# Performance work log

Measured on AMD Instinct MI355X. Metric: run time of the kernel, lower is better.

Reference implementation:

```python
import jax, jax.numpy as jnp
import numpy as np

N_NODES = 4096
EMB_DIM = 512
N_HEADS = 8
K_SPARSE = 128
HEAD_DIM = EMB_DIM // N_HEADS


def setup_inputs() -> dict:
    key = jax.random.key(0)
    k1, k2, k3, k4 = jax.random.split(key, 4)
    # xavier_uniform bound for square [D, D] weight
    bound = float(np.sqrt(6.0 / (EMB_DIM + EMB_DIM)))
    return {
        "embedding_matrix": jax.random.normal(k1, (N_NODES, EMB_DIM), dtype=jnp.float32),
        "Wq": jax.random.uniform(k2, (EMB_DIM, EMB_DIM), minval=-bound, maxval=bound, dtype=jnp.float32),
        "bq": jnp.zeros((EMB_DIM,), dtype=jnp.float32),
        "Wk": jax.random.uniform(k3, (EMB_DIM, EMB_DIM), minval=-bound, maxval=bound, dtype=jnp.float32),
        "bk": jnp.zeros((EMB_DIM,), dtype=jnp.float32),
        "sparse_indices": jax.random.randint(k4, (N_HEADS, N_NODES, K_SPARSE), 0, N_NODES, dtype=jnp.int32),
    }


def reference(embedding_matrix, Wq, bq, Wk, bk, sparse_indices):
    N, D = embedding_matrix.shape
    H, _, K = sparse_indices.shape
    hd = D // H
    # torch Linear: y = x @ W.T + b
    q = (embedding_matrix @ Wq.T + bq).reshape(N, H, hd).transpose(1, 0, 2)  # [H, N, hd]
    kk = (embedding_matrix @ Wk.T + bk).reshape(N, H, hd).transpose(1, 0, 2)  # [H, N, hd]
    # per-head gather of K random keys per query node: [H, N, K, hd]
    sel = jax.vmap(lambda kh, ih: kh[ih])(kk, sparse_indices)
    scores = jnp.einsum("hnd,hnkd->hnk", q, sel) / jnp.sqrt(jnp.float32(hd))  # [H, N, K]
    h_idx = jnp.arange(H)[:, None, None]
    n_idx = jnp.arange(N)[None, :, None]
    out = jnp.zeros((H, N, N), dtype=scores.dtype).at[h_idx, n_idx, sparse_indices].set(scores)
    return out
```

## Files before the change

kernel.cpp:

```cpp
#include <hip/hip_runtime.h>
#include <hip/hip_bf16.h>
#include <stdint.h>

#define N_NODES  4096
#define EMB_DIM  512
#define N_HEADS  8
#define K_SPARSE 128
#define HEAD_DIM 64

typedef __attribute__((ext_vector_type(8))) __bf16 bf16x8;
typedef __attribute__((ext_vector_type(4))) float  f32x4;

__device__ __forceinline__ float bf2f(unsigned short u) {
    union { unsigned int i; float f; } v;
    v.i = ((unsigned int)u) << 16;
    return v.f;
}

__device__ __forceinline__ unsigned short f2bf(float f) {
    union { float f; unsigned int i; } v;
    v.f = f;
    unsigned int x = v.i;
    unsigned int rounding = 0x7fffu + ((x >> 16) & 1u);
    x += rounding;
    return (unsigned short)(x >> 16);
}

__global__ __launch_bounds__(256) void proj_kernel(
    const float* __restrict__ X,
    const float* __restrict__ Wq, const float* __restrict__ bq,
    const float* __restrict__ Wk, const float* __restrict__ bk,
    unsigned short* __restrict__ Qb, unsigned short* __restrict__ Kb)
{
    __shared__ unsigned short As[64][40];
    __shared__ unsigned short Bs[128][40];

    const float* __restrict__ W    = blockIdx.z ? Wk : Wq;
    const float* __restrict__ bias = blockIdx.z ? bk : bq;
    unsigned short* __restrict__ out = blockIdx.z ? Kb : Qb;

    const int t    = threadIdx.x;
    const int M0   = blockIdx.x * 64;
    const int N0   = blockIdx.y * 128;
    const int lane = t & 63;
    const int wave = t >> 6;
    const int wm   = (wave >> 1) * 32;
    const int wn   = (wave & 1) * 64;

    const int arow = t >> 2;
    const int acol = (t & 3) * 8;
    const int brow = t >> 1;
    const int bcol = (t & 1) * 16;

    f32x4 acc[2][4] = {};

    for (int kt = 0; kt < EMB_DIM / 32; ++kt) {
        const int k0 = kt * 32;
        {
            const float4* srcA = (const float4*)(X + (size_t)(M0 + arow) * EMB_DIM + k0 + acol);
            float4 va0 = srcA[0], va1 = srcA[1];
            unsigned int pa[4];
            pa[0] = (unsigned int)f2bf(va0.x) | ((unsigned int)f2bf(va0.y) << 16);
            pa[1] = (unsigned int)f2bf(va0.z) | ((unsigned int)f2bf(va0.w) << 16);
            pa[2] = (unsigned int)f2bf(va1.x) | ((unsigned int)f2bf(va1.y) << 16);
            pa[3] = (unsigned int)f2bf(va1.z) | ((unsigned int)f2bf(va1.w) << 16);
            *(uint4*)&As[arow][acol] = make_uint4(pa[0], pa[1], pa[2], pa[3]);

            const float4* srcB = (const float4*)(W + (size_t)(N0 + brow) * EMB_DIM + k0 + bcol);
            unsigned int pb[8];
            #pragma unroll
            for (int c = 0; c < 4; ++c) {
                float4 vb = srcB[c];
                pb[c * 2 + 0] = (unsigned int)f2bf(vb.x) | ((unsigned int)f2bf(vb.y) << 16);
                pb[c * 2 + 1] = (unsigned int)f2bf(vb.z) | ((unsigned int)f2bf(vb.w) << 16);
            }
            uint4* dstB = (uint4*)&Bs[brow][bcol];
            dstB[0] = make_uint4(pb[0], pb[1], pb[2], pb[3]);
            dstB[1] = make_uint4(pb[4], pb[5], pb[6], pb[7]);
        }
        __syncthreads();

        bf16x8 af[2], bff[4];
        #pragma unroll
        for (int i = 0; i < 2; ++i)
            af[i] = __builtin_bit_cast(bf16x8,
                *(const uint4*)&As[wm + i * 16 + (lane & 15)][(lane >> 4) * 8]);
        #pragma unroll
        for (int i = 0; i < 4; ++i)
            bff[i] = __builtin_bit_cast(bf16x8,
                *(const uint4*)&Bs[wn + i * 16 + (lane & 15)][(lane >> 4) * 8]);

        #pragma unroll
        for (int mi = 0; mi < 2; ++mi)
            #pragma unroll
            for (int ni = 0; ni < 4; ++ni)
                acc[mi][ni] = __builtin_amdgcn_mfma_f32_16x16x32_bf16(
                    af[mi], bff[ni], acc[mi][ni], 0, 0, 0);
        __syncthreads();
    }

    #pragma unroll
    for (int mi = 0; mi < 2; ++mi) {
        #pragma unroll
        for (int ni = 0; ni < 4; ++ni) {
            const int col = N0 + wn + ni * 16 + (lane & 15);
            const float bval = bias[col];
            #pragma unroll
            for (int r = 0; r < 4; ++r) {
                const int row = M0 + wm + mi * 16 + (lane >> 4) * 4 + r;
                out[(size_t)row * EMB_DIM + col] = f2bf(acc[mi][ni][r] + bval);
            }
        }
    }
}

__global__ __launch_bounds__(64) void scatter_kernel(
    const unsigned short* __restrict__ Qb,
    const unsigned short* __restrict__ Kb,
    const int* __restrict__ sidx,
    float* __restrict__ out)
{
    __shared__ float rowbuf[N_NODES];

    const int t = threadIdx.x;
    const int b = blockIdx.x;
    const int h = b >> 12;
    const int n = b & (N_NODES - 1);
    const int j = t & 7;
    const int g = t >> 3;

    const int myIdx0 = sidx[(size_t)b * K_SPARSE + t];
    const int myIdx1 = sidx[(size_t)b * K_SPARSE + 64 + t];
    const uint4 qu = *(const uint4*)(Qb + (size_t)n * EMB_DIM + h * HEAD_DIM + j * 8);

    f32x4* rowv = (f32x4*)rowbuf;
    const f32x4 z4 = {0.0f, 0.0f, 0.0f, 0.0f};
    #pragma unroll
    for (int i = 0; i < 16; ++i) rowv[t + 64 * i] = z4;

    float q[8];
    {
        unsigned int uu[4] = {qu.x, qu.y, qu.z, qu.w};
        #pragma unroll
        for (int w = 0; w < 4; ++w) {
            q[2 * w + 0] = bf2f((unsigned short)(uu[w] & 0xffffu));
            q[2 * w + 1] = bf2f((unsigned short)(uu[w] >> 16));
        }
    }

    unsigned int* tags = (unsigned int*)rowbuf;
    asm volatile("s_waitcnt lgkmcnt(0)" ::: "memory");
    atomicMax(&tags[myIdx0], (unsigned int)(t + 1));
    atomicMax(&tags[myIdx1], (unsigned int)(t + 65));

    float score[16];
    int   kidx[16];
    #pragma unroll
    for (int p = 0; p < 16; ++p) {
        const int kk  = g + 8 * p;
        const int idx = (p < 8) ? __shfl(myIdx0, kk) : __shfl(myIdx1, kk - 64);
        kidx[p] = idx;
        const uint4 u = *(const uint4*)(Kb + (size_t)idx * EMB_DIM + h * HEAD_DIM + j * 8);
        unsigned int uu[4] = {u.x, u.y, u.z, u.w};
        float acc = 0.0f;
        #pragma unroll
        for (int w = 0; w < 4; ++w) {
            acc += bf2f((unsigned short)(uu[w] & 0xffffu)) * q[2 * w + 0];
            acc += bf2f((unsigned short)(uu[w] >> 16))     * q[2 * w + 1];
        }
        acc += __shfl_xor(acc, 1);
        acc += __shfl_xor(acc, 2);
        acc += __shfl_xor(acc, 4);
        score[p] = acc * 0.125f;
    }

    asm volatile("s_waitcnt lgkmcnt(0)" ::: "memory");
    if (j == 0) {
        unsigned int winmask = 0;
        #pragma unroll
        for (int p = 0; p < 16; ++p)
            if (tags[kidx[p]] == (unsigned int)(g + 8 * p + 1)) winmask |= (1u << p);
        asm volatile("s_waitcnt lgkmcnt(0)" ::: "memory");
        #pragma unroll
        for (int p = 0; p < 16; ++p)
            if (winmask & (1u << p)) rowbuf[kidx[p]] = score[p];
    }
    asm volatile("s_waitcnt lgkmcnt(0)" ::: "memory");

    f32x4* orowv = (f32x4*)(out + (size_t)b * N_NODES);
    #pragma unroll
    for (int i = 0; i < 16; ++i) {
        f32x4 v = rowv[t + 64 * i];
        __builtin_nontemporal_store(v, &orowv[t + 64 * i]);
    }
}

extern "C" void kernel_launch(void* const* d_in, const int* in_sizes, int n_in,
                              void* d_out, int out_size, void* d_ws, size_t ws_size,
                              hipStream_t stream) {
    const float* emb = (const float*)d_in[0];
    const float* Wq  = (const float*)d_in[1];
    const float* bq  = (const float*)d_in[2];
    const float* Wk  = (const float*)d_in[3];
    const float* bk  = (const float*)d_in[4];
    const int*   si  = (const int*)d_in[5];
    float* out = (float*)d_out;

    unsigned short* Qb = (unsigned short*)d_ws;
    unsigned short* Kb = Qb + (size_t)N_NODES * EMB_DIM;

    dim3 pg(N_NODES / 64, EMB_DIM / 128, 2);
    proj_kernel<<<pg, 256, 0, stream>>>(emb, Wq, bq, Wk, bk, Qb, Kb);

    scatter_kernel<<<N_HEADS * N_NODES, 64, 0, stream>>>(Qb, Kb, si, out);
}
```

Before: 579.6 us.

## Make scatter kernel persistent over 16 rows with software-pipelined gathers

The scatter kernel now uses 256-thread blocks that each process 16 consecutive output rows in a loop, instead of one 64-thread block per row. Key gathers and the index and query loads for the next rows are prefetched while the current row is written out, so load latency overlaps with the row stores. This cuts launch and scheduling overhead and hides gather latency. In exchange it adds several block-wide barriers per row, and each row's LDS zero/fill/readback is serialized within the block, which can reduce parallelism.

Result: slower. 620.1 us (+7.0%).

```diff
diff --git a/kernel.cpp b/kernel.cpp
--- a/kernel.cpp
+++ b/kernel.cpp
@@ -7,6 +7,9 @@
 #define N_HEADS  8
 #define K_SPARSE 128
 #define HEAD_DIM 64
+
+#define ROWS_PER_BLOCK 16
+#define SCATTER_BLOCKS (N_HEADS * N_NODES / ROWS_PER_BLOCK)
 
 typedef __attribute__((ext_vector_type(8))) __bf16 bf16x8;
 typedef __attribute__((ext_vector_type(4))) float  f32x4;
@@ -24,6 +27,12 @@
     unsigned int rounding = 0x7fffu + ((x >> 16) & 1u);
     x += rounding;
     return (unsigned short)(x >> 16);
+}
+
+__device__ __forceinline__ void lds_barrier() {
+    asm volatile("s_waitcnt lgkmcnt(0)" ::: "memory");
+    __builtin_amdgcn_s_barrier();
+    asm volatile("" ::: "memory");
 }
 
 __global__ __launch_bounds__(256) void proj_kernel(
@@ -114,84 +123,139 @@
     }
 }
 
-__global__ __launch_bounds__(64) void scatter_kernel(
+__global__ __launch_bounds__(256, 6) void scatter_kernel(
     const unsigned short* __restrict__ Qb,
     const unsigned short* __restrict__ Kb,
     const int* __restrict__ sidx,
     float* __restrict__ out)
 {
     __shared__ float rowbuf[N_NODES];
+    __shared__ int   sIdx[K_SPARSE];
 
     const int t = threadIdx.x;
-    const int b = blockIdx.x;
-    const int h = b >> 12;
-    const int n = b & (N_NODES - 1);
     const int j = t & 7;
-    const int g = t >> 3;
-
-    const int myIdx0 = sidx[(size_t)b * K_SPARSE + t];
-    const int myIdx1 = sidx[(size_t)b * K_SPARSE + 64 + t];
-    const uint4 qu = *(const uint4*)(Qb + (size_t)n * EMB_DIM + h * HEAD_DIM + j * 8);
-
+    const int base = blockIdx.x * ROWS_PER_BLOCK;
+
+    unsigned int* tags = (unsigned int*)rowbuf;
     f32x4* rowv = (f32x4*)rowbuf;
     const f32x4 z4 = {0.0f, 0.0f, 0.0f, 0.0f};
+
+    int sid_cur = 0;
+    if (t < K_SPARSE) sid_cur = sidx[(size_t)base * K_SPARSE + t];
+    uint4 qu_cur = *(const uint4*)(Qb + (size_t)(base & (N_NODES - 1)) * EMB_DIM
+                                   + (base >> 12) * HEAD_DIM + j * 8);
+
     #pragma unroll
-    for (int i = 0; i < 16; ++i) rowv[t + 64 * i] = z4;
-
-    float q[8];
+    for (int i2 = 0; i2 < 4; ++i2) rowv[t + 256 * i2] = z4;
+    if (t < K_SPARSE) sIdx[t] = sid_cur;
+    lds_barrier();
+
+    if (t < K_SPARSE) atomicMax(&tags[sid_cur], (unsigned int)(t + 1));
+
+    int  kidx[4];
+    uint4 u[4];
     {
-        unsigned int uu[4] = {qu.x, qu.y, qu.z, qu.w};
-        #pragma unroll
-        for (int w = 0; w < 4; ++w) {
-            q[2 * w + 0] = bf2f((unsigned short)(uu[w] & 0xffffu));
-            q[2 * w + 1] = bf2f((unsigned short)(uu[w] >> 16));
-        }
-    }
-
-    unsigned int* tags = (unsigned int*)rowbuf;
-    asm volatile("s_waitcnt lgkmcnt(0)" ::: "memory");
-    atomicMax(&tags[myIdx0], (unsigned int)(t + 1));
-    atomicMax(&tags[myIdx1], (unsigned int)(t + 65));
-
-    float score[16];
-    int   kidx[16];
-    #pragma unroll
-    for (int p = 0; p < 16; ++p) {
-        const int kk  = g + 8 * p;
-        const int idx = (p < 8) ? __shfl(myIdx0, kk) : __shfl(myIdx1, kk - 64);
-        kidx[p] = idx;
-        const uint4 u = *(const uint4*)(Kb + (size_t)idx * EMB_DIM + h * HEAD_DIM + j * 8);
-        unsigned int uu[4] = {u.x, u.y, u.z, u.w};
-        float acc = 0.0f;
-        #pragma unroll
-        for (int w = 0; w < 4; ++w) {
-            acc += bf2f((unsigned short)(uu[w] & 0xffffu)) * q[2 * w + 0];
-            acc += bf2f((unsigned short)(uu[w] >> 16))     * q[2 * w + 1];
-        }
-        acc += __shfl_xor(acc, 1);
-        acc += __shfl_xor(acc, 2);
-        acc += __shfl_xor(acc, 4);
-        score[p] = acc * 0.125f;
-    }
-
-    asm volatile("s_waitcnt lgkmcnt(0)" ::: "memory");
-    if (j == 0) {
+        const int h0 = base >> 12;
+        #pragma unroll
+        for (int p = 0; p < 4; ++p) {
+            const int kk = (t >> 3) + 32 * p;
+            kidx[p] = sIdx[kk];
+            u[p] = *(const uint4*)(Kb + (size_t)kidx[p] * EMB_DIM + h0 * HEAD_DIM + j * 8);
+        }
+    }
+
+    int sid_nxt = 0;
+    {
+        const int r1 = base + 1;
+        if (t < K_SPARSE) sid_nxt = sidx[(size_t)r1 * K_SPARSE + t];
+    }
+    uint4 qu_nxt = *(const uint4*)(Qb + (size_t)((base + 1) & (N_NODES - 1)) * EMB_DIM
+                                   + ((base + 1) >> 12) * HEAD_DIM + j * 8);
+
+    #pragma unroll 1
+    for (int i = 0; i < ROWS_PER_BLOCK; ++i) {
+        const int r = base + i;
+
+        float q[8];
+        {
+            unsigned int uu[4] = {qu_cur.x, qu_cur.y, qu_cur.z, qu_cur.w};
+            #pragma unroll
+            for (int w = 0; w < 4; ++w) {
+                q[2 * w + 0] = bf2f((unsigned short)(uu[w] & 0xffffu));
+                q[2 * w + 1] = bf2f((unsigned short)(uu[w] >> 16));
+            }
+        }
+        float score[4];
+        #pragma unroll
+        for (int p = 0; p < 4; ++p) {
+            unsigned int uu[4] = {u[p].x, u[p].y, u[p].z, u[p].w};
+            float acc = 0.0f;
+            #pragma unroll
+            for (int w = 0; w < 4; ++w) {
+                acc += bf2f((unsigned short)(uu[w] & 0xffffu)) * q[2 * w + 0];
+                acc += bf2f((unsigned short)(uu[w] >> 16))     * q[2 * w + 1];
+            }
+            acc += __shfl_xor(acc, 1);
+            acc += __shfl_xor(acc, 2);
+            acc += __shfl_xor(acc, 4);
+            score[p] = acc * 0.125f;
+        }
+
+        lds_barrier();
         unsigned int winmask = 0;
-        #pragma unroll
-        for (int p = 0; p < 16; ++p)
-            if (tags[kidx[p]] == (unsigned int)(g + 8 * p + 1)) winmask |= (1u << p);
-        asm volatile("s_waitcnt lgkmcnt(0)" ::: "memory");
-        #pragma unroll
-        for (int p = 0; p < 16; ++p)
-            if (winmask & (1u << p)) rowbuf[kidx[p]] = score[p];
-    }
-    asm volatile("s_waitcnt lgkmcnt(0)" ::: "memory");
-
-    f32x4* orowv = (f32x4*)(out + (size_t)b * N_NODES);
-    #pragma unroll
-    for (int i = 0; i < 16; ++i) {
-        f32x4 v = rowv[t + 64 * i];
-        __builtin_nontemporal_store(v, &orowv[t + 64 * i]);
+        if (j == 0) {
+            #pragma unroll
+            for (int p = 0; p < 4; ++p) {
+                const int kk = (t >> 3) + 32 * p;
+                if (tags[kidx[p]] == (unsigned int)(kk + 1)) winmask |= (1u << p);
+            }
+        }
+        lds_barrier();
+        if (j == 0) {
+            #pragma unroll
+            for (int p = 0; p < 4; ++p)
+                if (winmask & (1u << p)) rowbuf[kidx[p]] = score[p];
+        }
+        lds_barrier();
+
+        f32x4 v0 = rowv[t];
+        f32x4 v1 = rowv[t + 256];
+        f32x4 v2 = rowv[t + 512];
+        f32x4 v3 = rowv[t + 768];
+        lds_barrier();
+
+        #pragma unroll
+        for (int i2 = 0; i2 < 4; ++i2) rowv[t + 256 * i2] = z4;
+        if (t < K_SPARSE) sIdx[t] = sid_nxt;
+        lds_barrier();
+
+        if (t < K_SPARSE) atomicMax(&tags[sid_nxt], (unsigned int)(t + 1));
+
+        const int in1 = (i + 1 < ROWS_PER_BLOCK) ? i + 1 : ROWS_PER_BLOCK - 1;
+        const int rn  = base + in1;
+        const int hn  = rn >> 12;
+        #pragma unroll
+        for (int p = 0; p < 4; ++p) {
+            const int kk = (t >> 3) + 32 * p;
+            kidx[p] = sIdx[kk];
+            u[p] = *(const uint4*)(Kb + (size_t)kidx[p] * EMB_DIM + hn * HEAD_DIM + j * 8);
+        }
+        const int in2 = (i + 2 < ROWS_PER_BLOCK) ? i + 2 : ROWS_PER_BLOCK - 1;
+        const int rf  = base + in2;
+        int sid_fut = 0;
+        if (t < K_SPARSE) sid_fut = sidx[(size_t)rf * K_SPARSE + t];
+        uint4 qu_fut = *(const uint4*)(Qb + (size_t)(rf & (N_NODES - 1)) * EMB_DIM
+                                       + (rf >> 12) * HEAD_DIM + j * 8);
+
+        __builtin_amdgcn_sched_barrier(0);
+
+        f32x4* orowv = (f32x4*)(out + (size_t)r * N_NODES);
+        __builtin_nontemporal_store(v0, &orowv[t]);
+        __builtin_nontemporal_store(v1, &orowv[t + 256]);
+        __builtin_nontemporal_store(v2, &orowv[t + 512]);
+        __builtin_nontemporal_store(v3, &orowv[t + 768]);
+
+        qu_cur = qu_nxt; qu_nxt = qu_fut; sid_nxt = sid_fut;
     }
 }
 
@@ -212,5 +276,5 @@
     dim3 pg(N_NODES / 64, EMB_DIM / 128, 2);
     proj_kernel<<<pg, 256, 0, stream>>>(emb, Wq, bq, Wk, bk, Qb, Kb);
 
-    scatter_kernel<<<N_HEADS * N_NODES, 64, 0, stream>>>(Qb, Kb, si, out);
-}
+    scatter_kernel<<<SCATTER_BLOCKS, 256, 0, stream>>>(Qb, Kb, si, out);
+}
```
